# Optimization experiments

Measured on AMD Instinct MI355X. Metric: run time of the kernel, lower is better.

## Reference

```python
import jax, jax.numpy as jnp
import numpy as np

N_SLOTS, KEY_DIM, VAL_DIM = 8192, 64, 64
B, S, TOPK = 8, 2048, 8


def setup_inputs() -> dict:
    key = jax.random.key(0)
    k1, k2, k3, k4, k5 = jax.random.split(key, 5)
    queries = jax.random.normal(k1, (B, S, KEY_DIM), dtype=jnp.float32)
    keys_mem = jax.random.normal(k2, (N_SLOTS, KEY_DIM), dtype=jnp.float32) * 0.02
    vals_mem = jax.random.normal(k3, (N_SLOTS, VAL_DIM), dtype=jnp.float32) * 0.02
    fast_vals = jax.random.normal(k4, (N_SLOTS, VAL_DIM), dtype=jnp.float32) * 0.01
    timestamps = jax.random.uniform(k5, (N_SLOTS,), dtype=jnp.float32)
    return {
        "queries": queries,
        "keys_mem": keys_mem,
        "vals_mem": vals_mem,
        "fast_vals": fast_vals,
        "timestamps": timestamps,
        "topk": TOPK,
    }


def reference(queries, keys_mem, vals_mem, fast_vals, timestamps, topk):
    # sim: [B, S, n_slots], scaled dot-product vs. memory keys
    scale = keys_mem.shape[1] ** (-0.5)
    sim = jnp.einsum("bsd,nd->bsn", queries, keys_mem) * scale
    # topk indices computed on detached scores (torch uses sim.detach())
    _, idx = jax.lax.top_k(jax.lax.stop_gradient(sim), topk)  # idx: [B, S, k]
    # gather topk similarities (torch does this via one-hot * sim; same math)
    sim_topk = jnp.take_along_axis(sim, idx, axis=-1)  # [B, S, k]
    # effective memory = slow + fast store; gather rows (torch: one_hot @ memory)
    effective_memory = vals_mem + fast_vals  # [n_slots, val_dim]
    gathered_vals = effective_memory[idx]  # [B, S, k, val_dim]
    attn_weights = jax.nn.softmax(sim_topk, axis=-1)  # [B, S, k]
    weighted_vals = gathered_vals * attn_weights[..., None]  # [B, S, k, val_dim]
    ts_retrieved = timestamps[idx]  # [B, S, k]
    return weighted_vals, idx, ts_retrieved
```

## Files before the change

kernel.cpp:

```cpp
#include <hip/hip_runtime.h>
#include <math.h>

#define NQ      16384
#define NSLOTS  8192
#define D       64
#define K       8

#define WV_ELEMS  (NQ * K * D)
#define IDX_OFF   (WV_ELEMS)
#define TSO_OFF   (IDX_OFF + NQ * K)

#define QPB_P   32
#define BLOCK_P 512
#define HALVES  2
#define SPW_P   (NSLOTS / HALVES / 8)
#define ITERS_P (SPW_P / 32)

#define QPB_R   8
#define BLOCK_R 256

#define POOL_SHORT_OFF 1572864
#define WS_NEED_NEW  (4u * 1024u * 1024u)
#define WS_NEED_OLD  (3u * 1024u * 1024u)

using short8   = __attribute__((ext_vector_type(8))) short;
using ushort8  = __attribute__((ext_vector_type(8))) unsigned short;
using bf16x8   = __attribute__((ext_vector_type(8))) __bf16;
using f32x4    = __attribute__((ext_vector_type(4))) float;

#define MFMA_BF16(A, B, C) __builtin_amdgcn_mfma_f32_16x16x32_bf16((A), (B), (C), 0, 0, 0)

__device__ __forceinline__ bf16x8 load_frag(const unsigned short* p) {
    short8 s = *reinterpret_cast<const short8*>(p);
    return __builtin_bit_cast(bf16x8, s);
}

__device__ __forceinline__ float packkey(float s, int code) {
    unsigned u = __float_as_uint(s) & 0xFFFFE000u;
    return __uint_as_float(u | (unsigned)code);
}

__device__ __forceinline__ void ins8(float (&tv)[8], float key) {
    float k2 = fmaxf(key, tv[0]);
    float o0 = fminf(tv[1], k2);
    float o1 = __builtin_amdgcn_fmed3f(tv[1], tv[2], k2);
    float o2 = __builtin_amdgcn_fmed3f(tv[2], tv[3], k2);
    float o3 = __builtin_amdgcn_fmed3f(tv[3], tv[4], k2);
    float o4 = __builtin_amdgcn_fmed3f(tv[4], tv[5], k2);
    float o5 = __builtin_amdgcn_fmed3f(tv[5], tv[6], k2);
    float o6 = __builtin_amdgcn_fmed3f(tv[6], tv[7], k2);
    float o7 = fmaxf(tv[7], k2);
    tv[0]=o0; tv[1]=o1; tv[2]=o2; tv[3]=o3; tv[4]=o4; tv[5]=o5; tv[6]=o6; tv[7]=o7;
}

__device__ __forceinline__ void cs(float& a, float& b) {
    const float lo = fminf(a, b), hi = fmaxf(a, b);
    a = lo; b = hi;
}
__device__ __forceinline__ void sort_bitonic8(float (&v)[8]) {
    cs(v[0],v[4]); cs(v[1],v[5]); cs(v[2],v[6]); cs(v[3],v[7]);
    cs(v[0],v[2]); cs(v[1],v[3]); cs(v[4],v[6]); cs(v[5],v[7]);
    cs(v[0],v[1]); cs(v[2],v[3]); cs(v[4],v[5]); cs(v[6],v[7]);
}

__device__ __forceinline__ void csu(unsigned long long& a, unsigned long long& b) {
    const bool lt = a < b;
    const unsigned long long lo = lt ? a : b;
    const unsigned long long hi = lt ? b : a;
    a = lo; b = hi;
}
__device__ __forceinline__ void sort_bitonic8_u64(unsigned long long (&v)[8]) {
    csu(v[0],v[4]); csu(v[1],v[5]); csu(v[2],v[6]); csu(v[3],v[7]);
    csu(v[0],v[2]); csu(v[1],v[3]); csu(v[4],v[6]); csu(v[5],v[7]);
    csu(v[0],v[1]); csu(v[2],v[3]); csu(v[4],v[5]); csu(v[6],v[7]);
}

__device__ __forceinline__ unsigned short f2bf(float f) {
    unsigned u = __float_as_uint(f);
    return (unsigned short)((u + 0x7FFFu + ((u >> 16) & 1u)) >> 16);
}

__global__ __launch_bounds__(256)
void conv_kernel(const float* __restrict__ q, const float* __restrict__ k,
                 unsigned short* __restrict__ ws) {
    const int t = blockIdx.x * blockDim.x + threadIdx.x;
    if (t < 262144) {
        float4 v = reinterpret_cast<const float4*>(q)[t];
        unsigned long long r =
              (unsigned long long)f2bf(v.x * 0.125f)
            | ((unsigned long long)f2bf(v.y * 0.125f) << 16)
            | ((unsigned long long)f2bf(v.z * 0.125f) << 32)
            | ((unsigned long long)f2bf(v.w * 0.125f) << 48);
        reinterpret_cast<unsigned long long*>(ws + 524288)[t] = r;
    } else if (t < 393216) {
        const int i = t - 262144;
        float4 v = reinterpret_cast<const float4*>(k)[i];
        unsigned long long r =
              (unsigned long long)f2bf(v.x)
            | ((unsigned long long)f2bf(v.y) << 16)
            | ((unsigned long long)f2bf(v.z) << 32)
            | ((unsigned long long)f2bf(v.w) << 48);
        reinterpret_cast<unsigned long long*>(ws)[i] = r;
    }
}

__global__ __launch_bounds__(BLOCK_P, 8)
void ltm_prefilter_kernel(const unsigned short* __restrict__ kb,
                          const unsigned short* __restrict__ qb,
                          unsigned short* __restrict__ poolu)
{
    __shared__ float candk[QPB_P][68];

    const int tid  = threadIdx.x;
    const int lane = tid & 63;
    const int w    = tid >> 6;
    const int row  = lane & 15;
    const int g    = lane >> 4;
    const int g4   = g * 4;
    const int koff = g * 8;
    const int bid  = blockIdx.x;
    const int qbase = (bid >> 1) * QPB_P;
    const int half  = bid & 1;

    const unsigned short* qpA = qb + (size_t)(qbase + row) * D + koff;
    const bf16x8 bA0 = load_frag(qpA);
    const bf16x8 bA1 = load_frag(qpA + 32);
    const bf16x8 bB0 = load_frag(qpA + 16 * D);
    const bf16x8 bB1 = load_frag(qpA + 16 * D + 32);

    float tvA[8], tvB[8];
    #pragma unroll
    for (int i = 0; i < 8; ++i) { tvA[i] = -INFINITY; tvB[i] = -INFINITY; }

    const int wbase = half * (NSLOTS / HALVES) + w * SPW_P;

    const unsigned short* kp0 = kb + (size_t)(wbase + row) * D + koff;
    bf16x8 a00 = load_frag(kp0);
    bf16x8 a01 = load_frag(kp0 + 32);
    bf16x8 a10 = load_frag(kp0 + 16 * D);
    bf16x8 a11 = load_frag(kp0 + 16 * D + 32);

    int codeA = 8191 - (wbase + g4);

    #pragma unroll 2
    for (int it = 0; it < ITERS_P; ++it) {
        const int snext = wbase + (it + 1) * 32;
        const unsigned short* np_ = kb + (size_t)(snext + row) * D + koff;
        bf16x8 n00 = load_frag(np_);
        bf16x8 n01 = load_frag(np_ + 32);
        bf16x8 n10 = load_frag(np_ + 16 * D);
        bf16x8 n11 = load_frag(np_ + 16 * D + 32);

        const f32x4 z = {0.f, 0.f, 0.f, 0.f};
        f32x4 c00 = MFMA_BF16(a00, bA0, z);  c00 = MFMA_BF16(a01, bA1, c00);
        f32x4 c01 = MFMA_BF16(a00, bB0, z);  c01 = MFMA_BF16(a01, bB1, c01);
        f32x4 c10 = MFMA_BF16(a10, bA0, z);  c10 = MFMA_BF16(a11, bA1, c10);
        f32x4 c11 = MFMA_BF16(a10, bB0, z);  c11 = MFMA_BF16(a11, bB1, c11);

        ins8(tvA, packkey(c00[0], codeA     ));
        ins8(tvA, packkey(c00[1], codeA -  1));
        ins8(tvA, packkey(c00[2], codeA -  2));
        ins8(tvA, packkey(c00[3], codeA -  3));
        ins8(tvA, packkey(c10[0], codeA - 16));
        ins8(tvA, packkey(c10[1], codeA - 17));
        ins8(tvA, packkey(c10[2], codeA - 18));
        ins8(tvA, packkey(c10[3], codeA - 19));
        ins8(tvB, packkey(c01[0], codeA     ));
        ins8(tvB, packkey(c01[1], codeA -  1));
        ins8(tvB, packkey(c01[2], codeA -  2));
        ins8(tvB, packkey(c01[3], codeA -  3));
        ins8(tvB, packkey(c11[0], codeA - 16));
        ins8(tvB, packkey(c11[1], codeA - 17));
        ins8(tvB, packkey(c11[2], codeA - 18));
        ins8(tvB, packkey(c11[3], codeA - 19));

        codeA -= 32;
        a00 = n00; a01 = n01; a10 = n10; a11 = n11;
    }

    {
        float sA[8], sB[8];
        #pragma unroll
        for (int j = 0; j < 8; ++j) {
            sA[j] = __shfl_xor(tvA[j], 32, 64);
            sB[j] = __shfl_xor(tvB[j], 32, 64);
        }
        float mA[8], mB[8];
        #pragma unroll
        for (int j = 0; j < 8; ++j) {
            mA[j] = fmaxf(tvA[j], sA[7 - j]);
            mB[j] = fmaxf(tvB[j], sB[7 - j]);
        }
        sort_bitonic8(mA);
        sort_bitonic8(mB);
        #pragma unroll
        for (int j = 0; j < 8; ++j) {
            sA[j] = __shfl_xor(mA[j], 16, 64);
            sB[j] = __shfl_xor(mB[j], 16, 64);
        }
        float fA[8], fB[8];
        #pragma unroll
        for (int j = 0; j < 8; ++j) {
            fA[j] = fmaxf(mA[j], sA[7 - j]);
            fB[j] = fmaxf(mB[j], sB[7 - j]);
        }
        sort_bitonic8(fA);
        sort_bitonic8(fB);
        if (g == 0) {
            #pragma unroll
            for (int j = 0; j < 8; ++j) {
                candk[row     ][w * 8 + j] = fA[j];
                candk[row + 16][w * 8 + j] = fB[j];
            }
        }
    }
    __syncthreads();

    if (tid < 256) {
        const int  ql = tid >> 3;
        const int  jj = tid & 7;
        const bool hi = (jj & 1) != 0;

        float v[8];
        #pragma unroll
        for (int i = 0; i < 8; ++i) v[i] = candk[ql][jj * 8 + i];

        {
            float sk[8], mk[8];
            #pragma unroll
            for (int i = 0; i < 8; ++i) sk[i] = __shfl_xor(v[i], 1, 64);
            #pragma unroll
            for (int i = 0; i < 8; ++i)
                mk[i] = hi ? fmaxf(v[i], sk[7 - i]) : fminf(v[i], sk[7 - i]);
            sort_bitonic8(mk);
            #pragma unroll
            for (int i = 0; i < 8; ++i) v[i] = mk[i];
        }
        #pragma unroll
        for (int rnd = 0; rnd < 2; ++rnd) {
            const int st = rnd ? 5 : 3;
            float sk[8], mk[8], sk2[8];
            #pragma unroll
            for (int i = 0; i < 8; ++i) sk[i] = __shfl_xor(v[i], st, 64);
            #pragma unroll
            for (int i = 0; i < 8; ++i) mk[i] = fmaxf(v[i], sk[7 - i]);
            #pragma unroll
            for (int i = 0; i < 8; ++i) sk2[i] = __shfl_xor(mk[i], 1, 64);
            #pragma unroll
            for (int i = 0; i < 8; ++i)
                mk[i] = hi ? fmaxf(mk[i], sk2[i]) : fminf(mk[i], sk2[i]);
            sort_bitonic8(mk);
            #pragma unroll
            for (int i = 0; i < 8; ++i) v[i] = mk[i];
        }
        if (jj < 2) {
            ushort8 o;
            #pragma unroll
            for (int i = 0; i < 8; ++i)
                o[i] = (unsigned short)(8191u - (__float_as_uint(v[i]) & 8191u));
            *reinterpret_cast<ushort8*>(
                poolu + ((size_t)(qbase + ql) * 32 + half * 16 + jj * 8)) = o;
        }
    }
}

__global__ __launch_bounds__(BLOCK_R, 8)
void ltm_rescore_kernel(const float* __restrict__ queries,
                        const float* __restrict__ keys_mem,
                        const float* __restrict__ vals_mem,
                        const float* __restrict__ fast_vals,
                        const float* __restrict__ timestamps,
                        const unsigned short* __restrict__ poolu,
                        float* __restrict__ out)
{
    const int tid = threadIdx.x;
    const int ql  = tid >> 5;
    const int l32 = tid & 31;
    const int sg  = l32 >> 2;
    const int ls4 = l32 & 3;
    const int q   = blockIdx.x * QPB_R + ql;

    float4 qv4[4];
    {
        const float4* qp = reinterpret_cast<const float4*>(queries) + (size_t)q * 16 + ls4 * 4;
        #pragma unroll
        for (int i = 0; i < 4; ++i) qv4[i] = qp[i];
    }

    unsigned long long kk[4];
    #pragma unroll
    for (int jt = 0; jt < 4; ++jt) {
        const int sid = poolu[(size_t)q * 32 + sg * 4 + jt];
        const float4* kp = reinterpret_cast<const float4*>(keys_mem) + (size_t)sid * 16 + ls4 * 4;
        float p = 0.f;
        #pragma unroll
        for (int i = 0; i < 4; ++i) {
            const float4 kc = kp[i];
            p = fmaf(qv4[i].x, kc.x, p);
            p = fmaf(qv4[i].y, kc.y, p);
            p = fmaf(qv4[i].z, kc.z, p);
            p = fmaf(qv4[i].w, kc.w, p);
        }
        p += __shfl_xor(p, 1, 64);
        p += __shfl_xor(p, 2, 64);
        const float s = p * 0.125f;
        const unsigned u  = __float_as_uint(s);
        const unsigned ou = (u & 0x80000000u) ? ~u : (u | 0x80000000u);
        kk[jt] = ((unsigned long long)ou << 13) | (unsigned)(8191 - sid);
    }
    csu(kk[0], kk[1]); csu(kk[2], kk[3]);
    csu(kk[0], kk[2]); csu(kk[1], kk[3]);
    csu(kk[1], kk[2]);
    unsigned long long tk[8];
    tk[0] = 0ull; tk[1] = 0ull; tk[2] = 0ull; tk[3] = 0ull;
    tk[4] = kk[0]; tk[5] = kk[1]; tk[6] = kk[2]; tk[7] = kk[3];

    #pragma unroll
    for (int st = 4; st <= 16; st <<= 1) {
        unsigned long long sk[8], mk[8];
        #pragma unroll
        for (int j = 0; j < 8; ++j) sk[j] = __shfl_xor(tk[j], st, 64);
        #pragma unroll
        for (int j = 0; j < 8; ++j) {
            const unsigned long long a = tk[j], b = sk[7 - j];
            mk[j] = a > b ? a : b;
        }
        sort_bitonic8_u64(mk);
        #pragma unroll
        for (int j = 0; j < 8; ++j) tk[j] = mk[j];
    }

    float wv[K]; int wi[K];
    #pragma unroll
    for (int r = 0; r < K; ++r) {
        const unsigned long long best = tk[7 - r];
        const int      sid = 8191 - (int)(best & 8191ull);
        const unsigned ou  = (unsigned)(best >> 13);
        const unsigned ub  = (ou & 0x80000000u) ? (ou & 0x7FFFFFFFu) : ~ou;
        wv[r] = __uint_as_float(ub);
        wi[r] = sid;
    }
    const float m = wv[0];
    float e[K]; float sum = 0.f;
    #pragma unroll
    for (int r = 0; r < K; ++r) { e[r] = expf(wv[r] - m); sum += e[r]; }
    const float inv = 1.f / sum;

    {
        const int   r   = l32 >> 2;
        const int   s4  = l32 & 3;
        const int   id  = wi[r];
        const float wgt = e[r] * inv;
        const float4* vp = reinterpret_cast<const float4*>(vals_mem)  + (size_t)id * 16 + s4 * 4;
        const float4* fp = reinterpret_cast<const float4*>(fast_vals) + (size_t)id * 16 + s4 * 4;
        float4* op = reinterpret_cast<float4*>(out) + ((size_t)(q * K + r)) * 16 + s4 * 4;
        #pragma unroll
        for (int i = 0; i < 4; ++i) {
            const float4 a = vp[i];
            const float4 b = fp[i];
            float4 c;
            c.x = (a.x + b.x) * wgt;
            c.y = (a.y + b.y) * wgt;
            c.z = (a.z + b.z) * wgt;
            c.w = (a.w + b.w) * wgt;
            op[i] = c;
        }
        if (l32 < 8) {
            out[IDX_OFF + (size_t)q * K + l32] = (float)wi[l32];
        } else if (l32 < 16) {
            const int r2 = l32 - 8;
            out[TSO_OFF + (size_t)q * K + r2] = timestamps[wi[r2]];
        }
    }
}

#define QPB    32
#define BLOCK  512
#define WAVES  8
#define SPW    (NSLOTS / WAVES)
#define ITERS  (SPW / 32)

__global__ __launch_bounds__(BLOCK, 4)
void ltm_mfma_kernel(const float* __restrict__ queries,
                     const float* __restrict__ keys_mem,
                     const float* __restrict__ vals_mem,
                     const float* __restrict__ fast_vals,
                     const float* __restrict__ timestamps,
                     const unsigned short* __restrict__ kb,
                     const unsigned short* __restrict__ qb,
                     float* __restrict__ out)
{
    __shared__ float candk[QPB][68];

    const int tid  = threadIdx.x;
    const int lane = tid & 63;
    const int w    = tid >> 6;
    const int row  = lane & 15;
    const int g    = lane >> 4;
    const int g4   = g * 4;
    const int koff = g * 8;
    const int qbase = blockIdx.x * QPB;

    const unsigned short* qpA = qb + (size_t)(qbase + row) * D + koff;
    const bf16x8 bA0 = load_frag(qpA);
    const bf16x8 bA1 = load_frag(qpA + 32);
    const bf16x8 bB0 = load_frag(qpA + 16 * D);
    const bf16x8 bB1 = load_frag(qpA + 16 * D + 32);

    float tvA[8], tvB[8];
    #pragma unroll
    for (int i = 0; i < 8; ++i) { tvA[i] = -INFINITY; tvB[i] = -INFINITY; }

    const int wbase = w * SPW;
    const unsigned short* kp0 = kb + (size_t)(wbase + row) * D + koff;
    bf16x8 a00 = load_frag(kp0);
    bf16x8 a01 = load_frag(kp0 + 32);
    bf16x8 a10 = load_frag(kp0 + 16 * D);
    bf16x8 a11 = load_frag(kp0 + 16 * D + 32);

    int codeA = 8191 - (wbase + g4);

    #pragma unroll 2
    for (int it = 0; it < ITERS; ++it) {
        const int snext = wbase + (it + 1) * 32;
        const unsigned short* np_ = kb + (size_t)(snext + row) * D + koff;
        bf16x8 n00 = load_frag(np_);
        bf16x8 n01 = load_frag(np_ + 32);
        bf16x8 n10 = load_frag(np_ + 16 * D);
        bf16x8 n11 = load_frag(np_ + 16 * D + 32);

        const f32x4 z = {0.f, 0.f, 0.f, 0.f};
        f32x4 c00 = MFMA_BF16(a00, bA0, z);  c00 = MFMA_BF16(a01, bA1, c00);
        f32x4 c01 = MFMA_BF16(a00, bB0, z);  c01 = MFMA_BF16(a01, bB1, c01);
        f32x4 c10 = MFMA_BF16(a10, bA0, z);  c10 = MFMA_BF16(a11, bA1, c10);
        f32x4 c11 = MFMA_BF16(a10, bB0, z);  c11 = MFMA_BF16(a11, bB1, c11);

        ins8(tvA, packkey(c00[0], codeA     ));
        ins8(tvA, packkey(c00[1], codeA -  1));
        ins8(tvA, packkey(c00[2], codeA -  2));
        ins8(tvA, packkey(c00[3], codeA -  3));
        ins8(tvA, packkey(c10[0], codeA - 16));
        ins8(tvA, packkey(c10[1], codeA - 17));
        ins8(tvA, packkey(c10[2], codeA - 18));
        ins8(tvA, packkey(c10[3], codeA - 19));
        ins8(tvB, packkey(c01[0], codeA     ));
        ins8(tvB, packkey(c01[1], codeA -  1));
        ins8(tvB, packkey(c01[2], codeA -  2));
        ins8(tvB, packkey(c01[3], codeA -  3));
        ins8(tvB, packkey(c11[0], codeA - 16));
        ins8(tvB, packkey(c11[1], codeA - 17));
        ins8(tvB, packkey(c11[2], codeA - 18));
        ins8(tvB, packkey(c11[3], codeA - 19));

        codeA -= 32;
        a00 = n00; a01 = n01; a10 = n10; a11 = n11;
    }

    {
        float sA[8], sB[8];
        #pragma unroll
        for (int j = 0; j < 8; ++j) {
            sA[j] = __shfl_xor(tvA[j], 32, 64);
            sB[j] = __shfl_xor(tvB[j], 32, 64);
        }
        float mA[8], mB[8];
        #pragma unroll
        for (int j = 0; j < 8; ++j) {
            mA[j] = fmaxf(tvA[j], sA[7 - j]);
            mB[j] = fmaxf(tvB[j], sB[7 - j]);
        }
        sort_bitonic8(mA);
        sort_bitonic8(mB);
        #pragma unroll
        for (int j = 0; j < 8; ++j) {
            sA[j] = __shfl_xor(mA[j], 16, 64);
            sB[j] = __shfl_xor(mB[j], 16, 64);
        }
        if (g == 0) {
            #pragma unroll
            for (int j = 0; j < 8; ++j) {
                candk[row     ][w * 8 + j] = fmaxf(mA[j], sA[7 - j]);
                candk[row + 16][w * 8 + j] = fmaxf(mB[j], sB[7 - j]);
            }
        }
    }
    __syncthreads();

    const int ql  = tid >> 4;
    const int l16 = tid & 15;
    const int sg  = l16 >> 2;
    const int ls4 = l16 & 3;
    const int q   = qbase + ql;

    float4 qv4[4];
    {
        const float4* qp = reinterpret_cast<const float4*>(queries) + (size_t)q * 16 + ls4 * 4;
        #pragma unroll
        for (int i = 0; i < 4; ++i) qv4[i] = qp[i];
    }

    unsigned long long tk[8];
    #pragma unroll
    for (int i = 0; i < 8; ++i) tk[i] = 0ull;

    #pragma unroll 4
    for (int jt = 0; jt < 16; ++jt) {
        const float fk  = candk[ql][sg * 16 + jt];
        const int   sid = 8191 - (int)(__float_as_uint(fk) & 8191u);
        const float4* kp = reinterpret_cast<const float4*>(keys_mem) + (size_t)sid * 16 + ls4 * 4;
        float p = 0.f;
        #pragma unroll
        for (int i = 0; i < 4; ++i) {
            const float4 kc = kp[i];
            p = fmaf(qv4[i].x, kc.x, p);
            p = fmaf(qv4[i].y, kc.y, p);
            p = fmaf(qv4[i].z, kc.z, p);
            p = fmaf(qv4[i].w, kc.w, p);
        }
        p += __shfl_xor(p, 1, 64);
        p += __shfl_xor(p, 2, 64);
        const float s = p * 0.125f;
        const unsigned u  = __float_as_uint(s);
        const unsigned ou = (u & 0x80000000u) ? ~u : (u | 0x80000000u);
        const unsigned long long key =
            ((unsigned long long)ou << 13) | (unsigned)(8191 - sid);
        if (key > tk[0]) {
            tk[0] = key;
            #pragma unroll
            for (int uu = 0; uu < 7; ++uu) {
                const bool sw = tk[uu] > tk[uu + 1];
                const unsigned long long x = sw ? tk[uu + 1] : tk[uu];
                const unsigned long long y = sw ? tk[uu]     : tk[uu + 1];
                tk[uu] = x; tk[uu + 1] = y;
            }
        }
    }

    #pragma unroll
    for (int st = 4; st <= 8; st <<= 1) {
        unsigned long long sk[8], mk[8];
        #pragma unroll
        for (int j = 0; j < 8; ++j) sk[j] = __shfl_xor(tk[j], st, 64);
        #pragma unroll
        for (int j = 0; j < 8; ++j) {
            const unsigned long long a = tk[j], b = sk[7 - j];
            mk[j] = a > b ? a : b;
        }
        sort_bitonic8_u64(mk);
        #pragma unroll
        for (int j = 0; j < 8; ++j) tk[j] = mk[j];
    }

    float wv[K]; int wi[K];
    #pragma unroll
    for (int r = 0; r < K; ++r) {
        const unsigned long long best = tk[7 - r];
        const int      sid = 8191 - (int)(best & 8191ull);
        const unsigned ou  = (unsigned)(best >> 13);
        const unsigned ub  = (ou & 0x80000000u) ? (ou & 0x7FFFFFFFu) : ~ou;
        wv[r] = __uint_as_float(ub);
        wi[r] = sid;
    }
    const float m = wv[0];
    float e[K]; float sum = 0.f;
    #pragma unroll
    for (int r = 0; r < K; ++r) { e[r] = expf(wv[r] - m); sum += e[r]; }
    const float inv = 1.f / sum;

    {
        const int   r   = l16 >> 1;
        const int   h   = l16 & 1;
        const int   id  = wi[r];
        const float wgt = e[r] * inv;
        const float4* vp = reinterpret_cast<const float4*>(vals_mem)  + (size_t)id * 16 + h * 8;
        const float4* fp = reinterpret_cast<const float4*>(fast_vals) + (size_t)id * 16 + h * 8;
        float4* op = reinterpret_cast<float4*>(out) + ((size_t)(q * K + r)) * 16 + h * 8;
        #pragma unroll
        for (int i = 0; i < 8; ++i) {
            const float4 a = vp[i];
            const float4 b = fp[i];
            float4 c;
            c.x = (a.x + b.x) * wgt;
            c.y = (a.y + b.y) * wgt;
            c.z = (a.z + b.z) * wgt;
            c.w = (a.w + b.w) * wgt;
            op[i] = c;
        }
        if (l16 < 8) {
            out[IDX_OFF + (size_t)q * K + l16] = (float)wi[l16];
        } else {
            const int r2 = l16 - 8;
            out[TSO_OFF + (size_t)q * K + r2] = timestamps[wi[r2]];
        }
    }
}

#define FQPB   32
#define FTPQ   8
#define FBLOCK 256
#define FTS    128
#define FLDK   68
#define FNTILES (NSLOTS / FTS)

__global__ __launch_bounds__(FBLOCK, 2)
void ltm_fused_kernel(const float* __restrict__ queries,
                      const float* __restrict__ keys_mem,
                      const float* __restrict__ vals_mem,
                      const float* __restrict__ fast_vals,
                      const float* __restrict__ timestamps,
                      float* __restrict__ out)
{
    __shared__ float kt[FTS * FLDK];
    __shared__ float candv[FQPB][FTPQ * K];
    __shared__ int   candi[FQPB][FTPQ * K];
    __shared__ float selw[FQPB][K];
    __shared__ int   seli[FQPB][K];

    const int tid = threadIdx.x;
    const int ql  = tid / FTPQ;
    const int sub = tid % FTPQ;
    const int q   = blockIdx.x * FQPB + ql;

    float4 qv[D / 4];
    {
        const float4* qp = reinterpret_cast<const float4*>(queries + (size_t)q * D);
        #pragma unroll
        for (int i = 0; i < D / 4; ++i) qv[i] = qp[i];
    }

    float tv[K]; int ti[K];
    #pragma unroll
    for (int i = 0; i < K; ++i) { tv[i] = -INFINITY; ti[i] = 0; }

    for (int tile = 0; tile < FNTILES; ++tile) {
        __syncthreads();
        {
            const float4* kg = reinterpret_cast<const float4*>(keys_mem + (size_t)tile * FTS * D);
            #pragma unroll
            for (int i = 0; i < (FTS * D / 4) / FBLOCK; ++i) {
                const int e = tid + i * FBLOCK;
                const int row = e >> 4;
                const int col = e & 15;
                *reinterpret_cast<float4*>(&kt[row * FLDK + col * 4]) = kg[e];
            }
        }
        __syncthreads();

        #pragma unroll 4
        for (int j = 0; j < FTS / FTPQ; ++j) {
            const int local = sub + j * FTPQ;
            const float* kr = &kt[local * FLDK];
            float4 a0 = make_float4(0.f, 0.f, 0.f, 0.f);
            float4 a1 = make_float4(0.f, 0.f, 0.f, 0.f);
            #pragma unroll
            for (int i = 0; i < D / 4; i += 2) {
                const float4 k0 = *reinterpret_cast<const float4*>(&kr[(i + 0) * 4]);
                const float4 k1 = *reinterpret_cast<const float4*>(&kr[(i + 1) * 4]);
                a0.x = fmaf(k0.x, qv[i].x, a0.x);   a0.y = fmaf(k0.y, qv[i].y, a0.y);
                a0.z = fmaf(k0.z, qv[i].z, a0.z);   a0.w = fmaf(k0.w, qv[i].w, a0.w);
                a1.x = fmaf(k1.x, qv[i+1].x, a1.x); a1.y = fmaf(k1.y, qv[i+1].y, a1.y);
                a1.z = fmaf(k1.z, qv[i+1].z, a1.z); a1.w = fmaf(k1.w, qv[i+1].w, a1.w);
            }
            float s = ((a0.x + a1.x) + (a0.y + a1.y)) + ((a0.z + a1.z) + (a0.w + a1.w));
            s *= 0.125f;
            const int gid = tile * FTS + local;
            if (s > tv[0]) {
                tv[0] = s; ti[0] = gid;
                #pragma unroll
                for (int u = 0; u < K - 1; ++u) {
                    const bool sw = tv[u] > tv[u + 1];
                    const float va = sw ? tv[u + 1] : tv[u];
                    const float vb = sw ? tv[u]     : tv[u + 1];
                    const int   ia = sw ? ti[u + 1] : ti[u];
                    const int   ib = sw ? ti[u]     : ti[u + 1];
                    tv[u] = va; tv[u + 1] = vb; ti[u] = ia; ti[u + 1] = ib;
                }
            }
        }
    }

    #pragma unroll
    for (int i = 0; i < K; ++i) {
        candv[ql][sub * K + i] = tv[i];
        candi[ql][sub * K + i] = ti[i];
    }
    __syncthreads();

    if (sub == 0) {
        float wv[K]; int wi[K];
        #pragma unroll
        for (int r = 0; r < K; ++r) {
            float bv = -INFINITY; int bi = 0x7fffffff; int bp = 0;
            for (int c = 0; c < FTPQ * K; ++c) {
                const float v = candv[ql][c];
                const int  id = candi[ql][c];
                if ((v > bv) || (v == bv && id < bi)) { bv = v; bi = id; bp = c; }
            }
            candv[ql][bp] = -INFINITY;
            wv[r] = bv; wi[r] = bi;
        }
        const float m = wv[0];
        float e[K]; float sum = 0.f;
        #pragma unroll
        for (int r = 0; r < K; ++r) { e[r] = expf(wv[r] - m); sum += e[r]; }
        const float inv = 1.f / sum;
        #pragma unroll
        for (int r = 0; r < K; ++r) { selw[ql][r] = e[r] * inv; seli[ql][r] = wi[r]; }
    }
    __syncthreads();

    {
        const int r = sub;
        const int id = seli[ql][r];
        const float w = selw[ql][r];
        const float4* vp = reinterpret_cast<const float4*>(vals_mem  + (size_t)id * D);
        const float4* fp = reinterpret_cast<const float4*>(fast_vals + (size_t)id * D);
        float4* op = reinterpret_cast<float4*>(out + (size_t)(q * K + r) * D);
        #pragma unroll
        for (int i = 0; i < D / 4; ++i) {
            const float4 a = vp[i];
            const float4 b = fp[i];
            float4 c;
            c.x = (a.x + b.x) * w; c.y = (a.y + b.y) * w;
            c.z = (a.z + b.z) * w; c.w = (a.w + b.w) * w;
            op[i] = c;
        }
        out[IDX_OFF + (size_t)q * K + r] = (float)id;
        out[TSO_OFF + (size_t)q * K + r] = timestamps[id];
    }
}

extern "C" void kernel_launch(void* const* d_in, const int* in_sizes, int n_in,
                              void* d_out, int out_size, void* d_ws, size_t ws_size,
                              hipStream_t stream) {
    (void)in_sizes; (void)n_in; (void)out_size;
    const float* queries    = (const float*)d_in[0];
    const float* keys_mem   = (const float*)d_in[1];
    const float* vals_mem   = (const float*)d_in[2];
    const float* fast_vals  = (const float*)d_in[3];
    const float* timestamps = (const float*)d_in[4];
    float* out = (float*)d_out;

    if (ws_size >= WS_NEED_NEW) {
        unsigned short* ws = (unsigned short*)d_ws;
        unsigned short* poolu = ws + POOL_SHORT_OFF;
        conv_kernel<<<1536, 256, 0, stream>>>(queries, keys_mem, ws);
        ltm_prefilter_kernel<<<(NQ / QPB_P) * HALVES, BLOCK_P, 0, stream>>>(
            ws , ws + 524288 , poolu);
        ltm_rescore_kernel<<<NQ / QPB_R, BLOCK_R, 0, stream>>>(
            queries, keys_mem, vals_mem, fast_vals, timestamps, poolu, out);
    } else if (ws_size >= WS_NEED_OLD) {
        unsigned short* ws = (unsigned short*)d_ws;
        conv_kernel<<<1536, 256, 0, stream>>>(queries, keys_mem, ws);
        ltm_mfma_kernel<<<NQ / QPB, BLOCK, 0, stream>>>(
            queries, keys_mem, vals_mem, fast_vals, timestamps,
            ws , ws + 524288 , out);
    } else {
        ltm_fused_kernel<<<NQ / FQPB, FBLOCK, 0, stream>>>(
            queries, keys_mem, vals_mem, fast_vals, timestamps, out);
    }
}
```

Baseline: 107.0 us.

## Pair adjacent slots in bf16 prefilter and rescore both slots in fp32

```diff
diff --git a/kernel.cpp b/kernel.cpp
--- a/kernel.cpp
+++ b/kernel.cpp
@@ -73,6 +73,14 @@
     csu(v[0],v[4]); csu(v[1],v[5]); csu(v[2],v[6]); csu(v[3],v[7]);
     csu(v[0],v[2]); csu(v[1],v[3]); csu(v[4],v[6]); csu(v[5],v[7]);
     csu(v[0],v[1]); csu(v[2],v[3]); csu(v[4],v[5]); csu(v[6],v[7]);
+}
+__device__ __forceinline__ void sort8_u64(unsigned long long (&v)[8]) {
+    csu(v[0],v[1]); csu(v[2],v[3]); csu(v[4],v[5]); csu(v[6],v[7]);
+    csu(v[0],v[2]); csu(v[1],v[3]); csu(v[4],v[6]); csu(v[5],v[7]);
+    csu(v[1],v[2]); csu(v[5],v[6]);
+    csu(v[0],v[4]); csu(v[1],v[5]); csu(v[2],v[6]); csu(v[3],v[7]);
+    csu(v[2],v[4]); csu(v[3],v[5]);
+    csu(v[1],v[2]); csu(v[3],v[4]); csu(v[5],v[6]);
 }
 
 __device__ __forceinline__ unsigned short f2bf(float f) {
@@ -157,22 +165,14 @@
         f32x4 c10 = MFMA_BF16(a10, bA0, z);  c10 = MFMA_BF16(a11, bA1, c10);
         f32x4 c11 = MFMA_BF16(a10, bB0, z);  c11 = MFMA_BF16(a11, bB1, c11);
 
-        ins8(tvA, packkey(c00[0], codeA     ));
-        ins8(tvA, packkey(c00[1], codeA -  1));
-        ins8(tvA, packkey(c00[2], codeA -  2));
-        ins8(tvA, packkey(c00[3], codeA -  3));
-        ins8(tvA, packkey(c10[0], codeA - 16));
-        ins8(tvA, packkey(c10[1], codeA - 17));
-        ins8(tvA, packkey(c10[2], codeA - 18));
-        ins8(tvA, packkey(c10[3], codeA - 19));
-        ins8(tvB, packkey(c01[0], codeA     ));
-        ins8(tvB, packkey(c01[1], codeA -  1));
-        ins8(tvB, packkey(c01[2], codeA -  2));
-        ins8(tvB, packkey(c01[3], codeA -  3));
-        ins8(tvB, packkey(c11[0], codeA - 16));
-        ins8(tvB, packkey(c11[1], codeA - 17));
-        ins8(tvB, packkey(c11[2], codeA - 18));
-        ins8(tvB, packkey(c11[3], codeA - 19));
+        ins8(tvA, fmaxf(packkey(c00[0], codeA     ), packkey(c00[1], codeA -  1)));
+        ins8(tvA, fmaxf(packkey(c00[2], codeA -  2), packkey(c00[3], codeA -  3)));
+        ins8(tvA, fmaxf(packkey(c10[0], codeA - 16), packkey(c10[1], codeA - 17)));
+        ins8(tvA, fmaxf(packkey(c10[2], codeA - 18), packkey(c10[3], codeA - 19)));
+        ins8(tvB, fmaxf(packkey(c01[0], codeA     ), packkey(c01[1], codeA -  1)));
+        ins8(tvB, fmaxf(packkey(c01[2], codeA -  2), packkey(c01[3], codeA -  3)));
+        ins8(tvB, fmaxf(packkey(c11[0], codeA - 16), packkey(c11[1], codeA - 17)));
+        ins8(tvB, fmaxf(packkey(c11[2], codeA - 18), packkey(c11[3], codeA - 19)));
 
         codeA -= 32;
         a00 = n00; a01 = n01; a10 = n10; a11 = n11;
@@ -287,33 +287,33 @@
         for (int i = 0; i < 4; ++i) qv4[i] = qp[i];
     }
 
-    unsigned long long kk[4];
+    unsigned long long tk[8];
     #pragma unroll
     for (int jt = 0; jt < 4; ++jt) {
-        const int sid = poolu[(size_t)q * 32 + sg * 4 + jt];
-        const float4* kp = reinterpret_cast<const float4*>(keys_mem) + (size_t)sid * 16 + ls4 * 4;
-        float p = 0.f;
-        #pragma unroll
-        for (int i = 0; i < 4; ++i) {
-            const float4 kc = kp[i];
-            p = fmaf(qv4[i].x, kc.x, p);
-            p = fmaf(qv4[i].y, kc.y, p);
-            p = fmaf(qv4[i].z, kc.z, p);
-            p = fmaf(qv4[i].w, kc.w, p);
-        }
-        p += __shfl_xor(p, 1, 64);
-        p += __shfl_xor(p, 2, 64);
-        const float s = p * 0.125f;
-        const unsigned u  = __float_as_uint(s);
-        const unsigned ou = (u & 0x80000000u) ? ~u : (u | 0x80000000u);
-        kk[jt] = ((unsigned long long)ou << 13) | (unsigned)(8191 - sid);
-    }
-    csu(kk[0], kk[1]); csu(kk[2], kk[3]);
-    csu(kk[0], kk[2]); csu(kk[1], kk[3]);
-    csu(kk[1], kk[2]);
-    unsigned long long tk[8];
-    tk[0] = 0ull; tk[1] = 0ull; tk[2] = 0ull; tk[3] = 0ull;
-    tk[4] = kk[0]; tk[5] = kk[1]; tk[6] = kk[2]; tk[7] = kk[3];
+        const int pe   = poolu[(size_t)q * 32 + sg * 4 + jt];
+        const int base = pe & ~1;
+        #pragma unroll
+        for (int hh = 0; hh < 2; ++hh) {
+            const int sid = base + hh;
+            const float4* kp = reinterpret_cast<const float4*>(keys_mem) + (size_t)sid * 16 + ls4 * 4;
+            float p = 0.f;
+            #pragma unroll
+            for (int i = 0; i < 4; ++i) {
+                const float4 kc = kp[i];
+                p = fmaf(qv4[i].x, kc.x, p);
+                p = fmaf(qv4[i].y, kc.y, p);
+                p = fmaf(qv4[i].z, kc.z, p);
+                p = fmaf(qv4[i].w, kc.w, p);
+            }
+            p += __shfl_xor(p, 1, 64);
+            p += __shfl_xor(p, 2, 64);
+            const float s = p * 0.125f;
+            const unsigned u  = __float_as_uint(s);
+            const unsigned ou = (u & 0x80000000u) ? ~u : (u | 0x80000000u);
+            tk[jt * 2 + hh] = ((unsigned long long)ou << 13) | (unsigned)(8191 - sid);
+        }
+    }
+    sort8_u64(tk);
 
     #pragma unroll
     for (int st = 4; st <= 16; st <<= 1) {
```

Result: slower. 117.5 us (+9.8%).
